# Kernel optimization log

Measured on AMD Instinct MI355X. Metric: run time of the kernel, lower is better.

## Reference

```python
import jax, jax.numpy as jnp
import numpy as np

B, S, D = 512, 500, 128
NQ, NC, NQD, NCD = 10000, 500, 100, 100

def _glorot(key, shape):
    fan_in, fan_out = shape[0], shape[1]
    lim = np.sqrt(6.0 / (fan_in + fan_out))
    return jax.random.uniform(key, shape, jnp.float32, -lim, lim)

def setup_inputs() -> dict:
    key = jax.random.key(0)
    ks = jax.random.split(key, 24)
    inp = {
        'question_seq': jax.random.randint(ks[0], (B, S), 0, NQ),
        'concept_seq': jax.random.randint(ks[1], (B, S), 0, NC),
        'question_diff_seq': jax.random.randint(ks[2], (B, S), 0, NQD),
        'concept_diff_seq': jax.random.randint(ks[3], (B, S), 0, NCD),
        'correct_seq': jax.random.randint(ks[4], (B, S), 0, 2),
        # embedding tables
        'Eq': jax.random.normal(ks[5], (NQ, D), jnp.float32),
        'Ec': jax.random.normal(ks[6], (NC, D), jnp.float32),
        'Eqd': jax.random.normal(ks[7], (NQD, D), jnp.float32),
        'Ecd': jax.random.normal(ks[8], (NCD, D), jnp.float32),
        'Ecorr': jax.random.normal(ks[9], (2, D), jnp.float32),
        # linear layers (stored as [in, out], y = x @ W + b)
        'Wx': _glorot(ks[10], (4 * D, D)), 'bx': jnp.zeros((D,), jnp.float32),
        'Wsdf1': _glorot(ks[11], (D, D)), 'bsdf1': jnp.zeros((D,), jnp.float32),
        'Wsdf2': _glorot(ks[12], (D, D)), 'bsdf2': jnp.zeros((D,), jnp.float32),
        'Wpka1': _glorot(ks[13], (2 * D, D)), 'bpka1': jnp.zeros((D,), jnp.float32),
        'Wpka2': _glorot(ks[14], (2 * D, D)), 'bpka2': jnp.zeros((D,), jnp.float32),
        'Wki': _glorot(ks[15], (4 * D, D)), 'bki': jnp.zeros((D,), jnp.float32),
        # xavier_uniform init of h_pre (torch nn.init.xavier_uniform_ on zeros(B, D))
        'h0': _glorot(ks[16], (B, D)),
    }
    return inp

def reference(question_seq, concept_seq, question_diff_seq, concept_diff_seq,
              correct_seq, Eq, Ec, Eqd, Ecd, Ecorr, Wx, bx,
              Wsdf1, bsdf1, Wsdf2, bsdf2, Wpka1, bpka1, Wpka2, bpka2,
              Wki, bki, h0):
    # embed all sequences: [B, S, D]
    qe = Eq[question_seq]
    ce = Ec[concept_seq]
    qde = Eqd[question_diff_seq]
    cde = Ecd[concept_diff_seq]
    co = Ecorr[correct_seq]
    # x_t = generate_x_MLP(concat(...)) precomputed for all timesteps
    x_all = jnp.concatenate([qe, ce, qde, cde], axis=-1) @ Wx + bx  # [B, S, D]

    # time-major slices for scan over t = 0 .. S-2
    tm = lambda a: jnp.swapaxes(a, 0, 1)  # [S, B, D]
    xs = (tm(x_all)[:-1], tm(x_all)[1:], tm(co)[:-1], tm(qde)[:-1], tm(cde)[:-1])

    def step(h_pre, inputs):
        x_t, x_next, co_t, qd_t, cd_t = inputs
        input_sdf = x_t - h_pre
        sdf = jax.nn.sigmoid(input_sdf @ Wsdf1 + bsdf1) * jnp.tanh(input_sdf @ Wsdf2 + bsdf2)
        input_pka = jnp.concatenate([sdf, co_t], axis=-1)
        pka = jax.nn.sigmoid(input_pka @ Wpka1 + bpka1) * jnp.tanh(input_pka @ Wpka2 + bpka2)
        input_ki = jnp.concatenate([h_pre, co_t, qd_t, cd_t], axis=-1)
        gamma = jax.nn.sigmoid(input_ki @ Wki + bki)
        h = gamma * h_pre + (1.0 - gamma) * pka
        y_t = jax.nn.sigmoid(jnp.sum(x_next * h, axis=-1))  # [B]
        return h, y_t

    _, ys = jax.lax.scan(step, h0, xs)  # ys: [S-1, B]
    # y[:, S-1] is never written in the original (stays 0)
    y = jnp.concatenate([ys.T, jnp.zeros((question_seq.shape[0], 1), jnp.float32)], axis=1)
    return y
```

## Files before the change

### kernel.cpp

```cpp
#include <hip/hip_runtime.h>
#include <hip/hip_bf16.h>
#include <cstdint>
#include <cstddef>

#define BB 512
#define SS 500
#define TT 499
#define NRB 128
#define L2E 1.4426950408889634f

typedef float  f32x4  __attribute__((ext_vector_type(4)));
typedef short  bf16x8 __attribute__((ext_vector_type(8)));

static constexpr size_t OFF_TXQ   = 0;
static constexpr size_t OFF_TXC   = 5120000;
static constexpr size_t OFF_TXQD  = 5376000;
static constexpr size_t OFF_TXCD  = 5427200;
static constexpr size_t OFF_TKIQD = 5478400;
static constexpr size_t OFF_TKICD = 5529600;
static constexpr size_t OFF_TKICO = 5580800;
static constexpr size_t OFF_TP1   = 5581824;
static constexpr size_t OFF_TP2   = 5582848;
static constexpr size_t OFF_TXQ2  = 5583872;
static constexpr size_t OFF_TXC2  = 10703872;
static constexpr size_t OFF_WFRAG = 10959872;
static constexpr size_t OFF_CPK   = 11123712;
static constexpr size_t OFF_XCD   = 11189248;
static constexpr size_t OFF_KIPRE = 143309824;
static constexpr size_t OFF_YPART = 275430400;
static constexpr size_t TOTAL_WS  = 283606016;

__device__ unsigned char g_fb[TOTAL_WS];

__device__ __forceinline__ unsigned short f2bf(float f) {
    union { float f; uint32_t u; } v; v.f = f;
    uint32_t u = v.u;
    uint32_t r = u + 0x7FFFu + ((u >> 16) & 1u);
    return (unsigned short)(r >> 16);
}
__device__ __forceinline__ float fsig(float z) {
    return __builtin_amdgcn_rcpf(1.0f + __expf(-z));
}
__device__ __forceinline__ uint32_t cvtpk(float lo, float hi) {
    uint32_t r;
    asm("v_cvt_pk_bf16_f32 %0, %1, %2" : "=v"(r) : "v"(lo), "v"(hi));
    return r;
}
__device__ __forceinline__ void bar_lgkm() {
    asm volatile("s_waitcnt lgkmcnt(0)" ::: "memory");
    __builtin_amdgcn_s_barrier();
}
__device__ __forceinline__ float sum16(float x) {
    int a = __float_as_int(x);
    int b = __builtin_amdgcn_update_dpp(a, a, 0xB1, 0xF, 0xF, false);
    float s = x + __int_as_float(b);
    int c = __float_as_int(s);
    int d = __builtin_amdgcn_update_dpp(c, c, 0x4E, 0xF, 0xF, false);
    s += __int_as_float(d);
    int e = __float_as_int(s);
    int f = __builtin_amdgcn_update_dpp(e, e, 0x141, 0xF, 0xF, false);
    s += __int_as_float(f);
    int gg = __float_as_int(s);
    int hh = __builtin_amdgcn_update_dpp(gg, gg, 0x140, 0xF, 0xF, false);
    return s + __int_as_float(hh);
}
__device__ __forceinline__ float sel4(f32x4 a, int g) {
    float x01 = (g & 1) ? a[1] : a[0];
    float x23 = (g & 1) ? a[3] : a[2];
    return (g & 2) ? x23 : x01;
}

__global__ __launch_bounds__(128) void k_tables(
    const float* __restrict__ Eq, const float* __restrict__ Ec,
    const float* __restrict__ Eqd, const float* __restrict__ Ecd,
    const float* __restrict__ Ecorr,
    const float* __restrict__ Wx,  const float* __restrict__ bx,
    const float* __restrict__ Wpka1, const float* __restrict__ bpka1,
    const float* __restrict__ Wpka2, const float* __restrict__ bpka2,
    const float* __restrict__ Wki, const float* __restrict__ bki,
    float* __restrict__ Txq, float* __restrict__ Txc,
    float* __restrict__ Txqd, float* __restrict__ Txcd,
    float* __restrict__ TkiQd, float* __restrict__ TkiCd, float* __restrict__ TkiCo,
    float* __restrict__ Tp1, float* __restrict__ Tp2)
{
    int blk = blockIdx.x;
    const float* A; const float* W; const float* bias = nullptr; float* out; int row;
    float oscale = 1.0f;
    if      (blk < 10000) { A = Eq;    row = blk;          W = Wx;              bias = bx;    out = Txq;  }
    else if (blk < 10500) { A = Ec;    row = blk - 10000;  W = Wx  + 128*128;                 out = Txc;  }
    else if (blk < 10600) { A = Eqd;   row = blk - 10500;  W = Wx  + 256*128;                 out = Txqd; }
    else if (blk < 10700) { A = Ecd;   row = blk - 10600;  W = Wx  + 384*128;                 out = Txcd; }
    else if (blk < 10800) { A = Eqd;   row = blk - 10700;  W = Wki + 256*128;                 out = TkiQd;}
    else if (blk < 10900) { A = Ecd;   row = blk - 10800;  W = Wki + 384*128;                 out = TkiCd;}
    else if (blk < 10902) { A = Ecorr; row = blk - 10900;  W = Wki + 128*128;   bias = bki;   out = TkiCo;}
    else if (blk < 10904) { A = Ecorr; row = blk - 10902;  W = Wpka1 + 128*128; bias = bpka1; out = Tp1;  oscale = -L2E; }
    else                  { A = Ecorr; row = blk - 10904;  W = Wpka2 + 128*128; bias = bpka2; out = Tp2;  oscale = -2.0f*L2E; }

    __shared__ float a[128];
    int c = threadIdx.x;
    a[c] = A[row * 128 + c];
    __syncthreads();
    float acc = bias ? bias[c] : 0.0f;
    #pragma unroll 8
    for (int k = 0; k < 128; ++k) acc += a[k] * W[k * 128 + c];
    out[row * 128 + c] = acc * oscale;
}

__global__ __launch_bounds__(128) void k_tables2(
    const float* __restrict__ Wki,
    const float* __restrict__ Txq, const float* __restrict__ Txc,
    const float* __restrict__ Txqd, const float* __restrict__ Txcd,
    float* __restrict__ Txq2, float* __restrict__ Txc2,
    float* __restrict__ TkiQd, float* __restrict__ TkiCd)
{
    int blk = blockIdx.x;
    const float* A; float* out; int row; bool accum;
    if      (blk < 10000) { A = Txq;  row = blk;          out = Txq2;  accum = false; }
    else if (blk < 10500) { A = Txc;  row = blk - 10000;  out = Txc2;  accum = false; }
    else if (blk < 10600) { A = Txqd; row = blk - 10500;  out = TkiQd; accum = true;  }
    else                  { A = Txcd; row = blk - 10600;  out = TkiCd; accum = true;  }
    __shared__ float a[128];
    int c = threadIdx.x;
    a[c] = A[row * 128 + c];
    __syncthreads();
    float acc = accum ? out[row * 128 + c] : 0.0f;
    #pragma unroll 8
    for (int k = 0; k < 128; ++k) acc += a[k] * Wki[k * 128 + c];
    out[row * 128 + c] = acc;
}

__global__ __launch_bounds__(64) void k_wfrag(
    const float* __restrict__ Wsdf1, const float* __restrict__ Wsdf2,
    const float* __restrict__ Wpka1, const float* __restrict__ Wpka2,
    const float* __restrict__ Wki, unsigned short* __restrict__ wfrag)
{
    int bid = blockIdx.x;
    int m = bid >> 5, w = (bid >> 2) & 7, kt = bid & 3;
    const float* W = (m == 0) ? Wsdf1 : (m == 1) ? Wsdf2 : (m == 2) ? Wpka1 : (m == 3) ? Wpka2 : Wki;
    float sgn = (m == 0) ? -L2E : (m == 1) ? -2.0f*L2E : (m == 2) ? -L2E : (m == 3) ? -2.0f*L2E : L2E;
    int l = threadIdx.x;
    int cc = w * 16 + (l & 15);
    int k0 = kt * 32 + ((l >> 4) << 3);
    unsigned short v[8];
    #pragma unroll
    for (int j = 0; j < 8; ++j) v[j] = f2bf(sgn * W[(size_t)(k0 + j) * 128 + cc]);
    unsigned short* dst = wfrag + ((( (size_t)m * 8 + w) * 4 + kt) * 64 + l) * 8;
    #pragma unroll
    for (int j = 0; j < 8; ++j) dst[j] = v[j];
}

__global__ __launch_bounds__(512) void k_gather(
    const int* __restrict__ qs, const int* __restrict__ cs,
    const int* __restrict__ qds, const int* __restrict__ cds, const int* __restrict__ corr,
    const float* __restrict__ Txq, const float* __restrict__ Txc,
    const float* __restrict__ Txqd, const float* __restrict__ Txcd,
    const float* __restrict__ Txq2, const float* __restrict__ Txc2,
    const float* __restrict__ TkiQd, const float* __restrict__ TkiCd, const float* __restrict__ TkiCo,
    float* __restrict__ xcd, float* __restrict__ kipre, unsigned char* __restrict__ cpk)
{
    int bid = blockIdx.x;
    int t = bid >> 7, rb = bid & 127;
    int tid = threadIdx.x;
    int g = (tid >> 4) & 3;
    int col = (tid >> 6) * 16 + (tid & 15);
    int b = rb * 4 + g;

    int iq  = qs  [(size_t)b * SS + t];
    int ic  = cs  [(size_t)b * SS + t];
    int iqd = qds [(size_t)b * SS + t];
    int icd = cds [(size_t)b * SS + t];
    int ico = corr[(size_t)b * SS + t];

    float x = Txq [(size_t)iq  * 128 + col] + Txc [(size_t)ic  * 128 + col]
            + Txqd[(size_t)iqd * 128 + col] + Txcd[(size_t)icd * 128 + col];
    float k = (Txq2 [(size_t)iq  * 128 + col] + Txc2 [(size_t)ic  * 128 + col]
             + TkiQd[(size_t)iqd * 128 + col] + TkiCd[(size_t)icd * 128 + col]
             + TkiCo[(size_t)ico * 128 + col]) * (-L2E);

    xcd  [(size_t)bid * 512 + tid] = x;
    kipre[(size_t)bid * 512 + tid] = k;

    if (tid == 0) {
        unsigned char bpk = 0;
        #pragma unroll
        for (int r = 0; r < 4; ++r)
            bpk |= (unsigned char)((corr[(size_t)(rb * 4 + r) * SS + t] & 1) << r);
        cpk[(size_t)rb * 512 + t] = bpk;
    }
}

__global__ __launch_bounds__(512, 2) void k_rec(
    const float* __restrict__ xcd, const float* __restrict__ kipre,
    const unsigned char* __restrict__ cpkg,
    const unsigned short* __restrict__ wfrag,
    const float* __restrict__ Tp1, const float* __restrict__ Tp2,
    const float* __restrict__ bsdf1, const float* __restrict__ bsdf2,
    const float* __restrict__ h0, float* __restrict__ ypart)
{
    int rb = blockIdx.x;
    int tid = threadIdx.x;
    int w = tid >> 6, l = tid & 63;
    int g = l >> 4, cl = l & 15;
    int col = w * 16 + cl;

    __shared__ __align__(16) unsigned short dbuf[512];
    __shared__ __align__(16) unsigned short sbuf[512];

    bf16x8 wf[5][4];
    #pragma unroll
    for (int m = 0; m < 5; ++m)
        #pragma unroll
        for (int kt = 0; kt < 4; ++kt)
            wf[m][kt] = *(const bf16x8*)(wfrag + ((((size_t)m * 8 + w) * 4 + kt) * 64 + l) * 8);

    float bs1 = bsdf1[col] * (-L2E);
    float bs2 = bsdf2[col] * (-2.0f * L2E);
    float tp1a = Tp1[col], tp1b = Tp1[128 + col];
    float tp2a = Tp2[col], tp2b = Tp2[128 + col];

    float h = h0[(size_t)(rb * 4 + g) * 128 + col];

    int wline = ((col >> 3) ^ (g << 1)) & 15;
    char* pdw = (char*)dbuf + g * 256 + wline * 16 + (col & 7) * 2;
    char* psw = (char*)sbuf + g * 256 + wline * 16 + (col & 7) * 2;
    const bf16x8* prd[4]; const bf16x8* prs[4];
    int rrow = cl & 3;
    #pragma unroll
    for (int kt = 0; kt < 4; ++kt) {
        int off = rrow * 256 + (((kt * 4 + g) ^ (rrow << 1)) & 15) * 16;
        prd[kt] = (const bf16x8*)((char*)dbuf + off);
        prs[kt] = (const bf16x8*)((char*)sbuf + off);
    }

    const size_t TSTR = (size_t)NRB * 512;
    const float* xp = xcd + (size_t)rb * 512 + tid;
    const float* kp = kipre + (size_t)rb * 512 + tid;
    const unsigned char* cp = cpkg + (size_t)rb * 512;

    float xn   = xp[TSTR];
    float xn2  = xp[2 * TSTR];
    float kip  = kp[0];
    float kip1 = kp[TSTR];
    unsigned char c0 = cp[0], c1v = cp[1];

    float* ypt = ypart + (size_t)(rb * 8 + w) * 4 + g;
    const size_t YSTR = (size_t)NRB * 8 * 4;
    bool ystore = (cl == 0);

    {
        float x0 = xp[0];
        uint32_t pk = cvtpk(x0 - h, x0 - h);
        *(unsigned short*)pdw = (unsigned short)pk;
    }
    bar_lgkm();

    #pragma unroll 2
    for (int t = 0; t < TT; ++t) {
        float xn3  = xp[(size_t)(t + 3) * TSTR];
        float kip2 = kp[(size_t)(t + 2) * TSTR];
        unsigned char c2v = cp[t + 2];

        f32x4 s1 = {bs1, bs1, bs1, bs1};
        f32x4 s2 = {bs2, bs2, bs2, bs2};
        f32x4 gd = {0.f, 0.f, 0.f, 0.f};
        #pragma unroll
        for (int kt = 0; kt < 4; ++kt) {
            bf16x8 df = *prd[kt];
            s1 = __builtin_amdgcn_mfma_f32_16x16x32_bf16(df, wf[0][kt], s1, 0, 0, 0);
            s2 = __builtin_amdgcn_mfma_f32_16x16x32_bf16(df, wf[1][kt], s2, 0, 0, 0);
            gd = __builtin_amdgcn_mfma_f32_16x16x32_bf16(df, wf[4][kt], gd, 0, 0, 0);
        }
        float s1v = sel4(s1, g), s2v = sel4(s2, g), gdv = sel4(gd, g);
        float gv = __builtin_amdgcn_rcpf(1.0f + __builtin_amdgcn_exp2f(gdv + kip));
        float e1 = __builtin_amdgcn_exp2f(s1v), e2 = __builtin_amdgcn_exp2f(s2v);
        float sdf = (1.0f - e2) * __builtin_amdgcn_rcpf((1.0f + e1) * (1.0f + e2));
        {
            uint32_t pk = cvtpk(sdf, sdf);
            *(unsigned short*)psw = (unsigned short)pk;
        }
        bar_lgkm();

        f32x4 p1 = {0.f, 0.f, 0.f, 0.f};
        f32x4 p2 = {0.f, 0.f, 0.f, 0.f};
        #pragma unroll
        for (int kt = 0; kt < 4; ++kt) {
            bf16x8 sf = *prs[kt];
            p1 = __builtin_amdgcn_mfma_f32_16x16x32_bf16(sf, wf[2][kt], p1, 0, 0, 0);
            p2 = __builtin_amdgcn_mfma_f32_16x16x32_bf16(sf, wf[3][kt], p2, 0, 0, 0);
        }
        float p1v = sel4(p1, g), p2v = sel4(p2, g);
        unsigned int myb = (((unsigned int)c0) >> g) & 1u;
        float t1 = myb ? tp1b : tp1a;
        float t2 = myb ? tp2b : tp2a;
        float e1p = __builtin_amdgcn_exp2f(p1v + t1), e2p = __builtin_amdgcn_exp2f(p2v + t2);
        float pka = (1.0f - e2p) * __builtin_amdgcn_rcpf((1.0f + e1p) * (1.0f + e2p));
        h = gv * (h - pka) + pka;

        {
            uint32_t pk = cvtpk(xn - h, xn - h);
            *(unsigned short*)pdw = (unsigned short)pk;
        }
        float yv = sum16(xn * h);
        if (ystore) ypt[0] = yv;
        ypt += YSTR;
        bar_lgkm();

        xn = xn2; xn2 = xn3; kip = kip1; kip1 = kip2; c0 = c1v; c1v = c2v;
    }
}

__global__ __launch_bounds__(256) void k_yfinal(const float* __restrict__ ypart, float* __restrict__ y)
{
    int id = blockIdx.x * 256 + threadIdx.x;
    if (id >= BB * SS) return;
    int b = id / SS, t = id - b * SS;
    if (t == TT) { y[id] = 0.0f; return; }
    int rb = b >> 2, r = b & 3;
    const float* base = ypart + ((size_t)t * NRB + rb) * 32 + r;
    float s = 0.0f;
    #pragma unroll
    for (int w = 0; w < 8; ++w) s += base[w * 4];
    y[id] = fsig(s);
}

extern "C" void kernel_launch(void* const* d_in, const int* in_sizes, int n_in,
                              void* d_out, int out_size, void* d_ws, size_t ws_size,
                              hipStream_t stream) {
    const int* qs    = (const int*)d_in[0];
    const int* cs    = (const int*)d_in[1];
    const int* qds   = (const int*)d_in[2];
    const int* cds   = (const int*)d_in[3];
    const int* corr  = (const int*)d_in[4];
    const float* Eq    = (const float*)d_in[5];
    const float* Ec    = (const float*)d_in[6];
    const float* Eqd   = (const float*)d_in[7];
    const float* Ecd   = (const float*)d_in[8];
    const float* Ecorr = (const float*)d_in[9];
    const float* Wx    = (const float*)d_in[10];
    const float* bx    = (const float*)d_in[11];
    const float* Wsdf1 = (const float*)d_in[12];
    const float* bsdf1 = (const float*)d_in[13];
    const float* Wsdf2 = (const float*)d_in[14];
    const float* bsdf2 = (const float*)d_in[15];
    const float* Wpka1 = (const float*)d_in[16];
    const float* bpka1 = (const float*)d_in[17];
    const float* Wpka2 = (const float*)d_in[18];
    const float* bpka2 = (const float*)d_in[19];
    const float* Wki   = (const float*)d_in[20];
    const float* bki   = (const float*)d_in[21];
    const float* h0    = (const float*)d_in[22];

    char* base;
    if (ws_size >= TOTAL_WS) {
        base = (char*)d_ws;
    } else {
        void* p = nullptr;
        hipGetSymbolAddress(&p, HIP_SYMBOL(g_fb));
        base = (char*)p;
    }

    float* Txq   = (float*)(base + OFF_TXQ);
    float* Txc   = (float*)(base + OFF_TXC);
    float* Txqd  = (float*)(base + OFF_TXQD);
    float* Txcd  = (float*)(base + OFF_TXCD);
    float* TkiQd = (float*)(base + OFF_TKIQD);
    float* TkiCd = (float*)(base + OFF_TKICD);
    float* TkiCo = (float*)(base + OFF_TKICO);
    float* Tp1   = (float*)(base + OFF_TP1);
    float* Tp2   = (float*)(base + OFF_TP2);
    float* Txq2  = (float*)(base + OFF_TXQ2);
    float* Txc2  = (float*)(base + OFF_TXC2);
    unsigned short* wfrag = (unsigned short*)(base + OFF_WFRAG);
    unsigned char*  cpk   = (unsigned char*)(base + OFF_CPK);
    float* xcd   = (float*)(base + OFF_XCD);
    float* kipre = (float*)(base + OFF_KIPRE);
    float* ypart = (float*)(base + OFF_YPART);

    k_tables<<<10906, 128, 0, stream>>>(Eq, Ec, Eqd, Ecd, Ecorr, Wx, bx,
                                        Wpka1, bpka1, Wpka2, bpka2, Wki, bki,
                                        Txq, Txc, Txqd, Txcd, TkiQd, TkiCd, TkiCo, Tp1, Tp2);
    k_tables2<<<10700, 128, 0, stream>>>(Wki, Txq, Txc, Txqd, Txcd, Txq2, Txc2, TkiQd, TkiCd);
    k_wfrag<<<160, 64, 0, stream>>>(Wsdf1, Wsdf2, Wpka1, Wpka2, Wki, wfrag);
    k_gather<<<SS * NRB, 512, 0, stream>>>(qs, cs, qds, cds, corr,
                                           Txq, Txc, Txqd, Txcd, Txq2, Txc2,
                                           TkiQd, TkiCd, TkiCo, xcd, kipre, cpk);
    k_rec<<<NRB, 512, 0, stream>>>(xcd, kipre, cpk, wfrag, Tp1, Tp2,
                                   bsdf1, bsdf2, h0, ypart);
    k_yfinal<<<(BB * SS + 255) / 256, 256, 0, stream>>>(ypart, (float*)d_out);
}
```

Baseline: 557.9 us.

## Split recurrence over 256 blocks of two batch rows each

The recurrent kernel now handles two batch rows per block instead of four, doubling the grid to 256 blocks so more compute units work on the sequential scan. The gather, y-partial layout and final reduction are reworked for two rows per block, and the LDS swizzle is adjusted to match. Each MFMA chain is split into two independent accumulators (even and odd K-tiles) to shorten the dependent chain on the critical per-step path. Half the MFMA rows now do redundant work, and per-step sync overhead is unchanged, so each block does the same matrix work for fewer useful rows.

```diff
diff --git a/kernel.cpp b/kernel.cpp
--- a/kernel.cpp
+++ b/kernel.cpp
@@ -6,7 +6,7 @@
 #define BB 512
 #define SS 500
 #define TT 499
-#define NRB 128
+#define NRB 256
 #define L2E 1.4426950408889634f
 
 typedef float  f32x4  __attribute__((ext_vector_type(4)));
@@ -25,10 +25,10 @@
 static constexpr size_t OFF_TXC2  = 10703872;
 static constexpr size_t OFF_WFRAG = 10959872;
 static constexpr size_t OFF_CPK   = 11123712;
-static constexpr size_t OFF_XCD   = 11189248;
-static constexpr size_t OFF_KIPRE = 143309824;
-static constexpr size_t OFF_YPART = 275430400;
-static constexpr size_t TOTAL_WS  = 283606016;
+static constexpr size_t OFF_XCD   = 11254784;
+static constexpr size_t OFF_KIPRE = 143375360;
+static constexpr size_t OFF_YPART = 275495936;
+static constexpr size_t TOTAL_WS  = 283671552;
 
 __device__ unsigned char g_fb[TOTAL_WS];
 
@@ -63,11 +63,6 @@
     int gg = __float_as_int(s);
     int hh = __builtin_amdgcn_update_dpp(gg, gg, 0x140, 0xF, 0xF, false);
     return s + __int_as_float(hh);
-}
-__device__ __forceinline__ float sel4(f32x4 a, int g) {
-    float x01 = (g & 1) ? a[1] : a[0];
-    float x23 = (g & 1) ? a[3] : a[2];
-    return (g & 2) ? x23 : x01;
 }
 
 __global__ __launch_bounds__(128) void k_tables(
@@ -149,7 +144,7 @@
     for (int j = 0; j < 8; ++j) dst[j] = v[j];
 }
 
-__global__ __launch_bounds__(512) void k_gather(
+__global__ __launch_bounds__(256) void k_gather(
     const int* __restrict__ qs, const int* __restrict__ cs,
     const int* __restrict__ qds, const int* __restrict__ cds, const int* __restrict__ corr,
     const float* __restrict__ Txq, const float* __restrict__ Txc,
@@ -159,11 +154,11 @@
     float* __restrict__ xcd, float* __restrict__ kipre, unsigned char* __restrict__ cpk)
 {
     int bid = blockIdx.x;
-    int t = bid >> 7, rb = bid & 127;
+    int t = bid >> 8, rb = bid & 255;
     int tid = threadIdx.x;
-    int g = (tid >> 4) & 3;
-    int col = (tid >> 6) * 16 + (tid & 15);
-    int b = rb * 4 + g;
+    int row = tid >> 7;
+    int col = tid & 127;
+    int b = rb * 2 + row;
 
     int iq  = qs  [(size_t)b * SS + t];
     int ic  = cs  [(size_t)b * SS + t];
@@ -177,14 +172,14 @@
              + TkiQd[(size_t)iqd * 128 + col] + TkiCd[(size_t)icd * 128 + col]
              + TkiCo[(size_t)ico * 128 + col]) * (-L2E);
 
-    xcd  [(size_t)bid * 512 + tid] = x;
-    kipre[(size_t)bid * 512 + tid] = k;
+    xcd  [(size_t)bid * 256 + tid] = x;
+    kipre[(size_t)bid * 256 + tid] = k;
 
     if (tid == 0) {
         unsigned char bpk = 0;
         #pragma unroll
-        for (int r = 0; r < 4; ++r)
-            bpk |= (unsigned char)((corr[(size_t)(rb * 4 + r) * SS + t] & 1) << r);
+        for (int r = 0; r < 2; ++r)
+            bpk |= (unsigned char)((corr[(size_t)(rb * 2 + r) * SS + t] & 1) << r);
         cpk[(size_t)rb * 512 + t] = bpk;
     }
 }
@@ -202,9 +197,11 @@
     int w = tid >> 6, l = tid & 63;
     int g = l >> 4, cl = l & 15;
     int col = w * 16 + cl;
-
-    __shared__ __align__(16) unsigned short dbuf[512];
-    __shared__ __align__(16) unsigned short sbuf[512];
+    int row = g & 1;
+    bool owner = (g < 2);
+
+    __shared__ __align__(16) unsigned short dbuf[256];
+    __shared__ __align__(16) unsigned short sbuf[256];
 
     bf16x8 wf[5][4];
     #pragma unroll
@@ -218,23 +215,23 @@
     float tp1a = Tp1[col], tp1b = Tp1[128 + col];
     float tp2a = Tp2[col], tp2b = Tp2[128 + col];
 
-    float h = h0[(size_t)(rb * 4 + g) * 128 + col];
-
-    int wline = ((col >> 3) ^ (g << 1)) & 15;
-    char* pdw = (char*)dbuf + g * 256 + wline * 16 + (col & 7) * 2;
-    char* psw = (char*)sbuf + g * 256 + wline * 16 + (col & 7) * 2;
+    float h = h0[(size_t)(rb * 2 + row) * 128 + col];
+
+    char* pdw = (char*)dbuf + row * 256 + ((col * 2) ^ (row << 6));
+    char* psw = (char*)sbuf + row * 256 + ((col * 2) ^ (row << 6));
     const bf16x8* prd[4]; const bf16x8* prs[4];
-    int rrow = cl & 3;
+    int rrow = cl & 1;
     #pragma unroll
     for (int kt = 0; kt < 4; ++kt) {
-        int off = rrow * 256 + (((kt * 4 + g) ^ (rrow << 1)) & 15) * 16;
+        int off = rrow * 256 + ((kt * 64 + g * 16) ^ (rrow << 6));
         prd[kt] = (const bf16x8*)((char*)dbuf + off);
         prs[kt] = (const bf16x8*)((char*)sbuf + off);
     }
 
-    const size_t TSTR = (size_t)NRB * 512;
-    const float* xp = xcd + (size_t)rb * 512 + tid;
-    const float* kp = kipre + (size_t)rb * 512 + tid;
+    const size_t TSTR = (size_t)NRB * 256;
+    int eidx = row * 128 + col;
+    const float* xp = xcd + (size_t)rb * 256 + eidx;
+    const float* kp = kipre + (size_t)rb * 256 + eidx;
     const unsigned char* cp = cpkg + (size_t)rb * 512;
 
     float xn   = xp[TSTR];
@@ -243,14 +240,14 @@
     float kip1 = kp[TSTR];
     unsigned char c0 = cp[0], c1v = cp[1];
 
-    float* ypt = ypart + (size_t)(rb * 8 + w) * 4 + g;
-    const size_t YSTR = (size_t)NRB * 8 * 4;
-    bool ystore = (cl == 0);
+    float* ypt = ypart + (size_t)rb * 16 + w * 2 + row;
+    const size_t YSTR = (size_t)NRB * 16;
+    bool ystore = (owner && cl == 0);
 
     {
         float x0 = xp[0];
         uint32_t pk = cvtpk(x0 - h, x0 - h);
-        *(unsigned short*)pdw = (unsigned short)pk;
+        if (owner) *(unsigned short*)pdw = (unsigned short)pk;
     }
     bar_lgkm();
 
@@ -260,36 +257,52 @@
         float kip2 = kp[(size_t)(t + 2) * TSTR];
         unsigned char c2v = cp[t + 2];
 
-        f32x4 s1 = {bs1, bs1, bs1, bs1};
-        f32x4 s2 = {bs2, bs2, bs2, bs2};
-        f32x4 gd = {0.f, 0.f, 0.f, 0.f};
-        #pragma unroll
-        for (int kt = 0; kt < 4; ++kt) {
-            bf16x8 df = *prd[kt];
-            s1 = __builtin_amdgcn_mfma_f32_16x16x32_bf16(df, wf[0][kt], s1, 0, 0, 0);
-            s2 = __builtin_amdgcn_mfma_f32_16x16x32_bf16(df, wf[1][kt], s2, 0, 0, 0);
-            gd = __builtin_amdgcn_mfma_f32_16x16x32_bf16(df, wf[4][kt], gd, 0, 0, 0);
+        f32x4 s1a = {bs1, bs1, bs1, bs1}, s1b = {0.f, 0.f, 0.f, 0.f};
+        f32x4 s2a = {bs2, bs2, bs2, bs2}, s2b = {0.f, 0.f, 0.f, 0.f};
+        f32x4 gda = {0.f, 0.f, 0.f, 0.f}, gdb = {0.f, 0.f, 0.f, 0.f};
+        {
+            bf16x8 d0 = *prd[0], d1 = *prd[1], d2 = *prd[2], d3 = *prd[3];
+            s1a = __builtin_amdgcn_mfma_f32_16x16x32_bf16(d0, wf[0][0], s1a, 0, 0, 0);
+            s2a = __builtin_amdgcn_mfma_f32_16x16x32_bf16(d0, wf[1][0], s2a, 0, 0, 0);
+            gda = __builtin_amdgcn_mfma_f32_16x16x32_bf16(d0, wf[4][0], gda, 0, 0, 0);
+            s1b = __builtin_amdgcn_mfma_f32_16x16x32_bf16(d2, wf[0][2], s1b, 0, 0, 0);
+            s2b = __builtin_amdgcn_mfma_f32_16x16x32_bf16(d2, wf[1][2], s2b, 0, 0, 0);
+            gdb = __builtin_amdgcn_mfma_f32_16x16x32_bf16(d2, wf[4][2], gdb, 0, 0, 0);
+            s1a = __builtin_amdgcn_mfma_f32_16x16x32_bf16(d1, wf[0][1], s1a, 0, 0, 0);
+            s2a = __builtin_amdgcn_mfma_f32_16x16x32_bf16(d1, wf[1][1], s2a, 0, 0, 0);
+            gda = __builtin_amdgcn_mfma_f32_16x16x32_bf16(d1, wf[4][1], gda, 0, 0, 0);
+            s1b = __builtin_amdgcn_mfma_f32_16x16x32_bf16(d3, wf[0][3], s1b, 0, 0, 0);
+            s2b = __builtin_amdgcn_mfma_f32_16x16x32_bf16(d3, wf[1][3], s2b, 0, 0, 0);
+            gdb = __builtin_amdgcn_mfma_f32_16x16x32_bf16(d3, wf[4][3], gdb, 0, 0, 0);
         }
-        float s1v = sel4(s1, g), s2v = sel4(s2, g), gdv = sel4(gd, g);
+        float s1v = (row ? s1a[1] : s1a[0]) + (row ? s1b[1] : s1b[0]);
+        float s2v = (row ? s2a[1] : s2a[0]) + (row ? s2b[1] : s2b[0]);
+        float gdv = (row ? gda[1] : gda[0]) + (row ? gdb[1] : gdb[0]);
         float gv = __builtin_amdgcn_rcpf(1.0f + __builtin_amdgcn_exp2f(gdv + kip));
         float e1 = __builtin_amdgcn_exp2f(s1v), e2 = __builtin_amdgcn_exp2f(s2v);
         float sdf = (1.0f - e2) * __builtin_amdgcn_rcpf((1.0f + e1) * (1.0f + e2));
         {
             uint32_t pk = cvtpk(sdf, sdf);
-            *(unsigned short*)psw = (unsigned short)pk;
+            if (owner) *(unsigned short*)psw = (unsigned short)pk;
         }
         bar_lgkm();
 
-        f32x4 p1 = {0.f, 0.f, 0.f, 0.f};
-        f32x4 p2 = {0.f, 0.f, 0.f, 0.f};
-        #pragma unroll
-        for (int kt = 0; kt < 4; ++kt) {
-            bf16x8 sf = *prs[kt];
-            p1 = __builtin_amdgcn_mfma_f32_16x16x32_bf16(sf, wf[2][kt], p1, 0, 0, 0);
-            p2 = __builtin_amdgcn_mfma_f32_16x16x32_bf16(sf, wf[3][kt], p2, 0, 0, 0);
+        f32x4 p1a = {0.f, 0.f, 0.f, 0.f}, p1b = {0.f, 0.f, 0.f, 0.f};
+        f32x4 p2a = {0.f, 0.f, 0.f, 0.f}, p2b = {0.f, 0.f, 0.f, 0.f};
+        {
+            bf16x8 f0 = *prs[0], f1 = *prs[1], f2 = *prs[2], f3 = *prs[3];
+            p1a = __builtin_amdgcn_mfma_f32_16x16x32_bf16(f0, wf[2][0], p1a, 0, 0, 0);
+            p2a = __builtin_amdgcn_mfma_f32_16x16x32_bf16(f0, wf[3][0], p2a, 0, 0, 0);
+            p1b = __builtin_amdgcn_mfma_f32_16x16x32_bf16(f2, wf[2][2], p1b, 0, 0, 0);
+            p2b = __builtin_amdgcn_mfma_f32_16x16x32_bf16(f2, wf[3][2], p2b, 0, 0, 0);
+            p1a = __builtin_amdgcn_mfma_f32_16x16x32_bf16(f1, wf[2][1], p1a, 0, 0, 0);
+            p2a = __builtin_amdgcn_mfma_f32_16x16x32_bf16(f1, wf[3][1], p2a, 0, 0, 0);
+            p1b = __builtin_amdgcn_mfma_f32_16x16x32_bf16(f3, wf[2][3], p1b, 0, 0, 0);
+            p2b = __builtin_amdgcn_mfma_f32_16x16x32_bf16(f3, wf[3][3], p2b, 0, 0, 0);
         }
-        float p1v = sel4(p1, g), p2v = sel4(p2, g);
-        unsigned int myb = (((unsigned int)c0) >> g) & 1u;
+        float p1v = (row ? p1a[1] : p1a[0]) + (row ? p1b[1] : p1b[0]);
+        float p2v = (row ? p2a[1] : p2a[0]) + (row ? p2b[1] : p2b[0]);
+        unsigned int myb = (((unsigned int)c0) >> row) & 1u;
         float t1 = myb ? tp1b : tp1a;
         float t2 = myb ? tp2b : tp2a;
         float e1p = __builtin_amdgcn_exp2f(p1v + t1), e2p = __builtin_amdgcn_exp2f(p2v + t2);
@@ -298,7 +311,7 @@
 
         {
             uint32_t pk = cvtpk(xn - h, xn - h);
-            *(unsigned short*)pdw = (unsigned short)pk;
+            if (owner) *(unsigned short*)pdw = (unsigned short)pk;
         }
         float yv = sum16(xn * h);
         if (ystore) ypt[0] = yv;
@@ -315,11 +328,11 @@
     if (id >= BB * SS) return;
     int b = id / SS, t = id - b * SS;
     if (t == TT) { y[id] = 0.0f; return; }
-    int rb = b >> 2, r = b & 3;
-    const float* base = ypart + ((size_t)t * NRB + rb) * 32 + r;
+    int rb = b >> 1, r = b & 1;
+    const float* base = ypart + (size_t)t * NRB * 16 + (size_t)rb * 16 + r;
     float s = 0.0f;
     #pragma unroll
-    for (int w = 0; w < 8; ++w) s += base[w * 4];
+    for (int w = 0; w < 8; ++w) s += base[w * 2];
     y[id] = fsig(s);
 }
 
@@ -381,7 +394,7 @@
                                         Txq, Txc, Txqd, Txcd, TkiQd, TkiCd, TkiCo, Tp1, Tp2);
     k_tables2<<<10700, 128, 0, stream>>>(Wki, Txq, Txc, Txqd, Txcd, Txq2, Txc2, TkiQd, TkiCd);
     k_wfrag<<<160, 64, 0, stream>>>(Wsdf1, Wsdf2, Wpka1, Wpka2, Wki, wfrag);
-    k_gather<<<SS * NRB, 512, 0, stream>>>(qs, cs, qds, cds, corr,
+    k_gather<<<SS * NRB, 256, 0, stream>>>(qs, cs, qds, cds, corr,
                                            Txq, Txc, Txqd, Txcd, Txq2, Txc2,
                                            TkiQd, TkiCd, TkiCo, xcd, kipre, cpk);
     k_rec<<<NRB, 512, 0, stream>>>(xcd, kipre, cpk, wfrag, Tp1, Tp2,
```

Result: no change. 550.0 us (-1.4%).
